# Kernel tuning notes

Hardware: AMD Instinct MI355X
Metric: run time of the kernel (lower is better)

## Reference

```python
import jax, jax.numpy as jnp
import numpy as np

E, F, H = 8, 4096, 2048  # num_experts, ffn_hidden_size, hidden_size
B, S, K = 2, 1024, 4     # batch, seq_len, top_k


def setup_inputs() -> dict:
    key = jax.random.key(0)
    ks = jax.random.split(key, 7)
    x = jax.random.normal(ks[0], (B, S, H), dtype=jnp.float32)
    weights = jax.random.uniform(ks[1], (B * S, E), dtype=jnp.float32)
    top_weights = jax.random.uniform(ks[2], (B * S, K), dtype=jnp.float32)
    top_experts = jax.random.randint(ks[3], (B * S, K), 0, E)
    w1 = jax.random.normal(ks[4], (E, F, H), dtype=jnp.float32) * 0.02
    v1 = jax.random.normal(ks[5], (E, F, H), dtype=jnp.float32) * 0.02
    w2 = jax.random.normal(ks[6], (E, F, H), dtype=jnp.float32) * 0.02
    return {"x": x, "weights": weights, "top_weights": top_weights,
            "top_experts": top_experts, "w1": w1, "v1": v1, "w2": w2}


def reference(x, weights, top_weights, top_experts, w1, v1, w2):
    # weights (router probs) is accepted but unused, matching the torch forward.
    bsz, q_len, hidden = x.shape
    xt = x.reshape(-1, hidden)  # [T, H]
    num_experts = w1.shape[0]
    # scale[t, e] = sum_k top_weights[t, k] * (top_experts[t, k] == e)
    onehot = jax.nn.one_hot(top_experts, num_experts, dtype=xt.dtype)  # [T, K, E]
    scale = jnp.einsum("tke,tk->te", onehot, top_weights)  # [T, E]
    out = jnp.zeros_like(xt)
    for e in range(num_experts):  # fixed small expert loop, dense+masked combine
        gate = xt @ w1[e].T          # [T, F]
        up = xt @ v1[e].T            # [T, F]
        h = jax.nn.silu(gate) * up   # DbrxExpertGLU
        out = out + (h @ w2[e]) * scale[:, e:e + 1]
    return out.reshape(bsz, q_len, hidden)
```

## Files before the change

kernel.cpp:

```cpp
#include <hip/hip_runtime.h>
#include <hip/hip_bf16.h>

#define NE 8
#define FF 4096
#define HH 2048
#define TT 2048
#define KTOP 4

typedef unsigned short u16;
typedef __attribute__((ext_vector_type(8))) short bf16x8;
typedef __attribute__((ext_vector_type(4))) float f32x4;

__device__ __forceinline__ u16 f2u(float f) {
  __hip_bfloat16 b = __float2bfloat16(f);
  return *reinterpret_cast<u16*>(&b);
}

__device__ __forceinline__ void gld16(void* lds, const void* g) {
  __builtin_amdgcn_global_load_lds(
      (const __attribute__((address_space(1))) void*)g,
      (__attribute__((address_space(3))) void*)lds, 16, 0, 0);
}

__global__ void k_build(const int* __restrict__ te, int* __restrict__ cnt,
                        int* __restrict__ tok, int* __restrict__ posmap) {
  const int e = blockIdx.x;
  const int tl = threadIdx.x;
  const int base = tl * 8;
  int mem[8];
  int my = 0;
  #pragma unroll
  for (int i = 0; i < 8; ++i) {
    const int t = base + i;
    bool m = false;
    #pragma unroll
    for (int k = 0; k < KTOP; ++k) m |= (te[t * KTOP + k] == e);
    mem[i] = m ? 1 : 0;
    my += mem[i];
  }
  __shared__ int s[256];
  s[tl] = my;
  __syncthreads();
  for (int off = 1; off < 256; off <<= 1) {
    int v = (tl >= off) ? s[tl - off] : 0;
    __syncthreads();
    s[tl] += v;
    __syncthreads();
  }
  int r = s[tl] - my;
  if (tl == 255) cnt[e] = s[255];
  #pragma unroll
  for (int i = 0; i < 8; ++i) {
    if (mem[i]) {
      const int t = base + i;
      tok[e * TT + r] = t;
      posmap[t * NE + e] = r;
      ++r;
    }
  }
}

__global__ void k_cast4(const float4* __restrict__ src, ushort4* __restrict__ dst, int n4) {
  int stride = gridDim.x * blockDim.x;
  for (int i = blockIdx.x * blockDim.x + threadIdx.x; i < n4; i += stride) {
    float4 f = src[i];
    ushort4 o;
    o.x = f2u(f.x); o.y = f2u(f.y); o.z = f2u(f.z); o.w = f2u(f.w);
    dst[i] = o;
  }
}

__global__ void k_tcast(const float* __restrict__ w2, u16* __restrict__ dst) {
  const int e = blockIdx.z;
  const float* src = w2 + (size_t)e * FF * HH;
  u16* d = dst + (size_t)e * HH * FF;
  __shared__ float tile[64][33];
  int h0 = blockIdx.x * 32;
  int f0 = blockIdx.y * 64;
  int tx = threadIdx.x, ty = threadIdx.y;
  #pragma unroll
  for (int i = 0; i < 8; ++i)
    tile[ty + i * 8][tx] = src[(size_t)(f0 + ty + i * 8) * HH + h0 + tx];
  __syncthreads();
  #pragma unroll
  for (int i = 0; i < 4; ++i) {
    const int hh = ty + i * 8;
    ushort2 o;
    o.x = f2u(tile[tx * 2][hh]);
    o.y = f2u(tile[tx * 2 + 1][hh]);
    *(ushort2*)&d[(size_t)(h0 + hh) * FF + f0 + tx * 2] = o;
  }
}

template<int MODE>
__global__ __launch_bounds__(512)
void gemm256(const u16* __restrict__ Aall, const u16* __restrict__ Ball,
             const int* __restrict__ cnt, void* __restrict__ Oall,
             const float* __restrict__ W1, const float* __restrict__ V1,
             const int* __restrict__ tok, const u16* __restrict__ Zp) {
  constexpr int KD  = (MODE == 0) ? HH : FF;
  constexpr int NTK = KD / 64;
  constexpr int NT  = (MODE == 0) ? 32 : 8;
  constexpr int NB  = (MODE == 0) ? 2 * FF : HH;

  const int nwg = gridDim.x;
  const int bid = blockIdx.x;
  const int swz = (bid & 7) * (nwg >> 3) + (bid >> 3);
  const int e   = swz / (8 * NT);
  const int rem = swz % (8 * NT);
  const int ntl = rem / 8;
  const int mt  = rem % 8;
  const int c = cnt[e];
  const int mcap = (c + 255) & ~255;
  if (mt * 256 >= mcap) return;

  __shared__ __align__(16) u16 smem[65536];
  const int tid  = threadIdx.x;
  const int lane = tid & 63;
  const int wave = tid >> 6;
  const int wm = wave >> 2;
  const int wn = wave & 3;

  const int tq = tid >> 2;
  const int tc = (((tid & 3) ^ ((tid >> 3) & 3)) << 3);

  const u16* pA0;
  const u16* pA1;
  if constexpr (MODE == 0) {
    const int r0 = mt * 256 + tq;
    const int r1 = r0 + 128;
    pA0 = ((r0 < c) ? Aall + (size_t)tok[e * TT + r0] * HH : Zp) + tc;
    pA1 = ((r1 < c) ? Aall + (size_t)tok[e * TT + r1] * HH : Zp) + tc;
  } else {
    const u16* A = Aall + (size_t)e * TT * KD + (size_t)(mt * 256) * KD;
    pA0 = A + (size_t)tq * KD + tc;
    pA1 = pA0 + (size_t)128 * KD;
  }

  auto stageA = [&](int d, int ks, int kt) {
    u16* dst = smem + ((d * 2 + ks) << 13) + tid * 8;
    const int off = kt * 64 + ks * 32;
    gld16(dst,        pA0 + off);
    gld16(dst + 4096, pA1 + off);
  };

  const u16* pB = Ball + (size_t)e * NB * KD + (size_t)(ntl * 256) * KD
                       + (size_t)tq * KD + tc;
  auto stageB = [&](int d, int ks, int kt) {
    u16* dst = smem + 32768 + ((d * 2 + ks) << 13) + tid * 8;
    const u16* src = pB + kt * 64 + ks * 32;
    gld16(dst,        src);
    gld16(dst + 4096, src + (size_t)128 * KD);
  };

  const float* pW = nullptr;
  if constexpr (MODE == 0) {
    const int sel = (tq >> 4) & 1;
    const int fr  = ntl * 128 + (tq >> 5) * 16 + (tq & 15);
    pW = (sel ? V1 : W1) + ((size_t)(e * FF + fr)) * HH + (tid & 3) * 8;
  }
  float4 br0[4], br1[4];
  auto issueB = [&](float4* br, int ks, int kt) {
    const float* s = pW + kt * 64 + ks * 32;
    br[0] = ((const float4*)s)[0];
    br[1] = ((const float4*)s)[1];
    const float* s2 = s + (size_t)64 * HH;
    br[2] = ((const float4*)s2)[0];
    br[3] = ((const float4*)s2)[1];
  };
  auto cvtB = [&](float4* br, int d, int ks) {
    u16* dst = smem + 32768 + ((d * 2 + ks) << 13) + tq * 32 + tc;
    union { ushort u[8]; bf16x8 v; } lo, hi;
    lo.u[0]=f2u(br[0].x); lo.u[1]=f2u(br[0].y); lo.u[2]=f2u(br[0].z); lo.u[3]=f2u(br[0].w);
    lo.u[4]=f2u(br[1].x); lo.u[5]=f2u(br[1].y); lo.u[6]=f2u(br[1].z); lo.u[7]=f2u(br[1].w);
    hi.u[0]=f2u(br[2].x); hi.u[1]=f2u(br[2].y); hi.u[2]=f2u(br[2].z); hi.u[3]=f2u(br[2].w);
    hi.u[4]=f2u(br[3].x); hi.u[5]=f2u(br[3].y); hi.u[6]=f2u(br[3].z); hi.u[7]=f2u(br[3].w);
    *(bf16x8*)(dst)        = lo.v;
    *(bf16x8*)(dst + 4096) = hi.v;
  };

  f32x4 acc[8][4];
  #pragma unroll
  for (int m = 0; m < 8; ++m)
    #pragma unroll
    for (int n = 0; n < 4; ++n)
      acc[m][n] = (f32x4){0.f, 0.f, 0.f, 0.f};

  const int lr = lane & 15;
  const int lc = ((((lane >> 4) & 3) ^ ((lane >> 1) & 3)) << 3);

  bf16x8 af[4], bf[4];
  auto rdA = [&](int d, int ks, int mq) {
    const u16* blk = smem + ((d * 2 + ks) << 13);
    #pragma unroll
    for (int m = 0; m < 4; ++m)
      af[m] = *(const bf16x8*)(blk + (wm * 128 + mq * 64 + m * 16 + lr) * 32 + lc);
  };
  auto rdB = [&](int d, int ks) {
    const u16* blk = smem + 32768 + ((d * 2 + ks) << 13);
    #pragma unroll
    for (int n = 0; n < 4; ++n)
      bf[n] = *(const bf16x8*)(blk + (wn * 64 + n * 16 + lr) * 32 + lc);
  };
  auto vmwait = [&](int n) {
    switch (n) {
      case 0:  asm volatile("s_waitcnt vmcnt(0)"  ::: "memory"); break;
      case 2:  asm volatile("s_waitcnt vmcnt(2)"  ::: "memory"); break;
      case 4:  asm volatile("s_waitcnt vmcnt(4)"  ::: "memory"); break;
      case 6:  asm volatile("s_waitcnt vmcnt(6)"  ::: "memory"); break;
      default: asm volatile("s_waitcnt vmcnt(8)"  ::: "memory"); break;
    }
  };
  auto MF = [&](int mq) {
    __builtin_amdgcn_s_setprio(1);
    #pragma unroll
    for (int m = 0; m < 4; ++m)
      #pragma unroll
      for (int n = 0; n < 4; ++n)
        acc[mq * 4 + m][n] = __builtin_amdgcn_mfma_f32_16x16x32_bf16(
            af[m], bf[n], acc[mq * 4 + m][n], 0, 0, 0);
    __builtin_amdgcn_s_setprio(0);
  };

  if constexpr (MODE == 0) {
    issueB(br0, 0, 0);
    issueB(br1, 1, 0);
    stageA(0, 0, 0);
    stageA(0, 1, 0);
    cvtB(br0, 0, 0);
    cvtB(br1, 0, 1);
    issueB(br0, 0, 1);
    issueB(br1, 1, 1);
    vmwait(8);
    asm volatile("s_waitcnt lgkmcnt(0)" ::: "memory");
  } else {
    stageA(0, 0, 0); stageB(0, 0, 0);
    stageA(0, 1, 0); stageB(0, 1, 0);
    stageA(1, 0, 1);
    vmwait(6);
  }
  __builtin_amdgcn_s_barrier();

  for (int t = 0; t < NTK; ++t) {
    const int d = t & 1, dn = d ^ 1;
    const bool hasN  = (t + 1 < NTK);
    const bool hasN2 = (t + 2 < NTK);
    rdB(d, 0); rdA(d, 0, 0);
    if constexpr (MODE == 0) { if (hasN) stageA(dn, 0, t + 1); }
    else                     { if (hasN) stageB(dn, 0, t + 1); }
    __builtin_amdgcn_s_barrier();
    asm volatile("s_waitcnt lgkmcnt(0)" ::: "memory");
    __builtin_amdgcn_sched_barrier(0);
    MF(0);
    __builtin_amdgcn_s_barrier();
    rdA(d, 0, 1);
    if (hasN) stageA(dn, 1, t + 1);
    __builtin_amdgcn_s_barrier();
    asm volatile("s_waitcnt lgkmcnt(0)" ::: "memory");
    __builtin_amdgcn_sched_barrier(0);
    MF(1);
    if constexpr (MODE == 1) {
      int v = 4 * NTK - 4 * t - 4; v = v > 3 ? 3 : (v < 0 ? 0 : v);
      vmwait(v * 2);
    }
    __builtin_amdgcn_s_barrier();
    rdB(d, 1); rdA(d, 1, 0);
    if constexpr (MODE == 1) { if (hasN) stageB(dn, 1, t + 1); }
    __builtin_amdgcn_s_barrier();
    asm volatile("s_waitcnt lgkmcnt(0)" ::: "memory");
    __builtin_amdgcn_sched_barrier(0);
    MF(0);
    if constexpr (MODE == 0) {
      if (hasN)  cvtB(br0, dn, 0);
      if (hasN2) issueB(br0, 0, t + 2);
    }
    __builtin_amdgcn_s_barrier();
    rdA(d, 1, 1);
    if constexpr (MODE == 1) { if (hasN2) stageA(d, 0, t + 2); }
    __builtin_amdgcn_s_barrier();
    asm volatile("s_waitcnt lgkmcnt(0)" ::: "memory");
    __builtin_amdgcn_sched_barrier(0);
    MF(1);
    if constexpr (MODE == 0) {
      if (hasN)  cvtB(br1, dn, 1);
      if (hasN2) issueB(br1, 1, t + 2);
      vmwait(hasN2 ? 8 : 0);
    } else {
      int v = 4 * NTK - 4 * t - 6; v = v > 3 ? 3 : (v < 0 ? 0 : v);
      vmwait(v * 2);
    }
    __builtin_amdgcn_s_barrier();
  }

  const int rb = mt * 256 + wm * 128 + ((lane >> 4) << 2);
  if (MODE == 0) {
    u16* H = (u16*)Oall + (size_t)e * TT * FF;
    const int fb = ntl * 128 + wn * 32 + lr;
    #pragma unroll
    for (int m = 0; m < 8; ++m)
      #pragma unroll
      for (int np = 0; np < 2; ++np)
        #pragma unroll
        for (int j = 0; j < 4; ++j) {
          float g = acc[m][2*np][j];
          float u = acc[m][2*np + 1][j];
          float hh = (g / (1.f + __expf(-g))) * u;
          H[(size_t)(rb + m*16 + j) * FF + fb + np*16] = f2u(hh);
        }
  } else {
    float* D = (float*)Oall + (size_t)e * TT * HH;
    const int cb = ntl * 256 + wn * 64 + lr;
    #pragma unroll
    for (int m = 0; m < 8; ++m)
      #pragma unroll
      for (int n = 0; n < 4; ++n)
        #pragma unroll
        for (int j = 0; j < 4; ++j)
          D[(size_t)(rb + m*16 + j) * HH + cb + n*16] = acc[m][n][j];
  }
}

__global__ void k_combine(const float* __restrict__ tw, const int* __restrict__ te,
                          const int* __restrict__ posmap, const float* __restrict__ dcomp,
                          float* __restrict__ out) {
  const int t = blockIdx.x;
  const int c0 = threadIdx.x * 8;
  float a[8] = {0.f, 0.f, 0.f, 0.f, 0.f, 0.f, 0.f, 0.f};
  #pragma unroll
  for (int k = 0; k < KTOP; ++k) {
    const int e = te[t * KTOP + k];
    const float w = tw[t * KTOP + k];
    const int r = posmap[t * NE + e];
    const float* row = dcomp + ((size_t)e * TT + r) * HH + c0;
    const float4 p = ((const float4*)row)[0];
    const float4 q = ((const float4*)row)[1];
    a[0] += w * p.x; a[1] += w * p.y; a[2] += w * p.z; a[3] += w * p.w;
    a[4] += w * q.x; a[5] += w * q.y; a[6] += w * q.z; a[7] += w * q.w;
  }
  float* o = out + (size_t)t * HH + c0;
  ((float4*)o)[0] = (float4){a[0], a[1], a[2], a[3]};
  ((float4*)o)[1] = (float4){a[4], a[5], a[6], a[7]};
}

extern "C" void kernel_launch(void* const* d_in, const int* in_sizes, int n_in,
                              void* d_out, int out_size, void* d_ws, size_t ws_size,
                              hipStream_t stream) {
  const float* x  = (const float*)d_in[0];
  const float* tw = (const float*)d_in[2];
  const int*   te = (const int*)d_in[3];
  const float* w1 = (const float*)d_in[4];
  const float* v1 = (const float*)d_in[5];
  const float* w2 = (const float*)d_in[6];
  float* out = (float*)d_out;

  char* p = (char*)d_ws;
  int*   cnt    = (int*)p;   p += 256;
  int*   tok    = (int*)p;   p += (size_t)NE * TT * 4;
  int*   posmap = (int*)p;   p += (size_t)TT * NE * 4;
  u16*   zp     = (u16*)p;   p += (size_t)HH * 2;
  u16*   xb     = (u16*)p;   p += (size_t)TT * HH * 2;
  u16*   w2tb   = (u16*)p;   p += (size_t)NE * HH * FF * 2;
  u16*   hc     = (u16*)p;   p += (size_t)NE * TT * FF * 2;
  float* dcomp  = (float*)p; p += (size_t)NE * TT * HH * 4;

  hipMemsetAsync(zp, 0, (size_t)HH * 2, stream);
  k_build<<<NE, 256, 0, stream>>>(te, cnt, tok, posmap);
  k_cast4<<<1024, 256, 0, stream>>>((const float4*)x, (ushort4*)xb, TT * HH / 4);
  k_tcast<<<dim3(HH / 32, FF / 64, NE), dim3(32, 8), 0, stream>>>(w2, w2tb);

  gemm256<0><<<2048, 512, 0, stream>>>(xb, w2tb, cnt, hc, w1, v1, tok, zp);
  gemm256<1><<<512, 512, 0, stream>>>(hc, w2tb, cnt, dcomp, nullptr, nullptr,
                                      nullptr, nullptr);
  k_combine<<<TT, 256, 0, stream>>>(tw, te, posmap, dcomp, out);
}
```

Measured before the change: 550.5 us.

## Fold W2 transpose-cast into GEMM1 launch and simplify main-loop barriers

```diff
diff --git a/kernel.cpp b/kernel.cpp
--- a/kernel.cpp
+++ b/kernel.cpp
@@ -10,6 +10,8 @@
 typedef unsigned short u16;
 typedef __attribute__((ext_vector_type(8))) short bf16x8;
 typedef __attribute__((ext_vector_type(4))) float f32x4;
+
+#define CFENCE asm volatile("" ::: "memory")
 
 __device__ __forceinline__ u16 f2u(float f) {
   __hip_bfloat16 b = __float2bfloat16(f);
@@ -70,42 +72,51 @@
   }
 }
 
-__global__ void k_tcast(const float* __restrict__ w2, u16* __restrict__ dst) {
-  const int e = blockIdx.z;
-  const float* src = w2 + (size_t)e * FF * HH;
-  u16* d = dst + (size_t)e * HH * FF;
-  __shared__ float tile[64][33];
-  int h0 = blockIdx.x * 32;
-  int f0 = blockIdx.y * 64;
-  int tx = threadIdx.x, ty = threadIdx.y;
-  #pragma unroll
-  for (int i = 0; i < 8; ++i)
-    tile[ty + i * 8][tx] = src[(size_t)(f0 + ty + i * 8) * HH + h0 + tx];
-  __syncthreads();
-  #pragma unroll
-  for (int i = 0; i < 4; ++i) {
-    const int hh = ty + i * 8;
-    ushort2 o;
-    o.x = f2u(tile[tx * 2][hh]);
-    o.y = f2u(tile[tx * 2 + 1][hh]);
-    *(ushort2*)&d[(size_t)(h0 + hh) * FF + f0 + tx * 2] = o;
-  }
-}
-
 template<int MODE>
 __global__ __launch_bounds__(512)
 void gemm256(const u16* __restrict__ Aall, const u16* __restrict__ Ball,
              const int* __restrict__ cnt, void* __restrict__ Oall,
              const float* __restrict__ W1, const float* __restrict__ V1,
-             const int* __restrict__ tok, const u16* __restrict__ Zp) {
+             const int* __restrict__ tok, const u16* __restrict__ Zp,
+             const float* __restrict__ W2, u16* __restrict__ W2t) {
   constexpr int KD  = (MODE == 0) ? HH : FF;
   constexpr int NTK = KD / 64;
   constexpr int NT  = (MODE == 0) ? 32 : 8;
   constexpr int NB  = (MODE == 0) ? 2 * FF : HH;
-
-  const int nwg = gridDim.x;
+  constexpr int NWG = (MODE == 0) ? 2048 : 512;
+
+  __shared__ __align__(16) u16 smem[65536];
   const int bid = blockIdx.x;
-  const int swz = (bid & 7) * (nwg >> 3) + (bid >> 3);
+  const int tid = threadIdx.x;
+
+  if (MODE == 0 && bid >= NWG) {
+    float (*tile)[65] = reinterpret_cast<float(*)[65]>(smem);
+    const int r = tid >> 3;
+    const int c0 = (tid & 7) * 8;
+    for (int i = 0; i < 8; ++i) {
+      const int g = (bid - NWG) * 8 + i;
+      const int e = g >> 11;
+      const int rem = g & 2047;
+      const int f0 = (rem >> 5) << 6;
+      const int h0 = (rem & 31) << 6;
+      const float* src = W2 + (size_t)e * FF * HH + (size_t)(f0 + r) * HH + h0 + c0;
+      float4 a = ((const float4*)src)[0];
+      float4 b = ((const float4*)src)[1];
+      tile[r][c0 + 0] = a.x; tile[r][c0 + 1] = a.y;
+      tile[r][c0 + 2] = a.z; tile[r][c0 + 3] = a.w;
+      tile[r][c0 + 4] = b.x; tile[r][c0 + 5] = b.y;
+      tile[r][c0 + 6] = b.z; tile[r][c0 + 7] = b.w;
+      __syncthreads();
+      union { ushort u[8]; bf16x8 v; } o;
+      #pragma unroll
+      for (int j = 0; j < 8; ++j) o.u[j] = f2u(tile[c0 + j][r]);
+      *(bf16x8*)(W2t + (size_t)e * HH * FF + (size_t)(h0 + r) * FF + f0 + c0) = o.v;
+      __syncthreads();
+    }
+    return;
+  }
+
+  const int swz = (bid & 7) * (NWG >> 3) + (bid >> 3);
   const int e   = swz / (8 * NT);
   const int rem = swz % (8 * NT);
   const int ntl = rem / 8;
@@ -114,8 +125,6 @@
   const int mcap = (c + 255) & ~255;
   if (mt * 256 >= mcap) return;
 
-  __shared__ __align__(16) u16 smem[65536];
-  const int tid  = threadIdx.x;
   const int lane = tid & 63;
   const int wave = tid >> 6;
   const int wm = wave >> 2;
@@ -205,8 +214,6 @@
   auto vmwait = [&](int n) {
     switch (n) {
       case 0:  asm volatile("s_waitcnt vmcnt(0)"  ::: "memory"); break;
-      case 2:  asm volatile("s_waitcnt vmcnt(2)"  ::: "memory"); break;
-      case 4:  asm volatile("s_waitcnt vmcnt(4)"  ::: "memory"); break;
       case 6:  asm volatile("s_waitcnt vmcnt(6)"  ::: "memory"); break;
       default: asm volatile("s_waitcnt vmcnt(8)"  ::: "memory"); break;
     }
@@ -234,62 +241,48 @@
     vmwait(8);
     asm volatile("s_waitcnt lgkmcnt(0)" ::: "memory");
   } else {
-    stageA(0, 0, 0); stageB(0, 0, 0);
-    stageA(0, 1, 0); stageB(0, 1, 0);
-    stageA(1, 0, 1);
-    vmwait(6);
+    stageA(0, 0, 0); stageA(0, 1, 0);
+    stageB(0, 0, 0); stageB(0, 1, 0);
+    vmwait(0);
   }
   __builtin_amdgcn_s_barrier();
+  CFENCE;
 
   for (int t = 0; t < NTK; ++t) {
     const int d = t & 1, dn = d ^ 1;
     const bool hasN  = (t + 1 < NTK);
     const bool hasN2 = (t + 2 < NTK);
+
     rdB(d, 0); rdA(d, 0, 0);
-    if constexpr (MODE == 0) { if (hasN) stageA(dn, 0, t + 1); }
-    else                     { if (hasN) stageB(dn, 0, t + 1); }
-    __builtin_amdgcn_s_barrier();
-    asm volatile("s_waitcnt lgkmcnt(0)" ::: "memory");
+    if (hasN) {
+      stageA(dn, 0, t + 1);
+      stageA(dn, 1, t + 1);
+      if constexpr (MODE == 1) { stageB(dn, 0, t + 1); stageB(dn, 1, t + 1); }
+    }
     __builtin_amdgcn_sched_barrier(0);
     MF(0);
-    __builtin_amdgcn_s_barrier();
     rdA(d, 0, 1);
-    if (hasN) stageA(dn, 1, t + 1);
-    __builtin_amdgcn_s_barrier();
-    asm volatile("s_waitcnt lgkmcnt(0)" ::: "memory");
-    __builtin_amdgcn_sched_barrier(0);
     MF(1);
-    if constexpr (MODE == 1) {
-      int v = 4 * NTK - 4 * t - 4; v = v > 3 ? 3 : (v < 0 ? 0 : v);
-      vmwait(v * 2);
-    }
-    __builtin_amdgcn_s_barrier();
-    rdB(d, 1); rdA(d, 1, 0);
-    if constexpr (MODE == 1) { if (hasN) stageB(dn, 1, t + 1); }
-    __builtin_amdgcn_s_barrier();
-    asm volatile("s_waitcnt lgkmcnt(0)" ::: "memory");
-    __builtin_amdgcn_sched_barrier(0);
-    MF(0);
     if constexpr (MODE == 0) {
       if (hasN)  cvtB(br0, dn, 0);
       if (hasN2) issueB(br0, 0, t + 2);
     }
-    __builtin_amdgcn_s_barrier();
-    rdA(d, 1, 1);
-    if constexpr (MODE == 1) { if (hasN2) stageA(d, 0, t + 2); }
-    __builtin_amdgcn_s_barrier();
-    asm volatile("s_waitcnt lgkmcnt(0)" ::: "memory");
-    __builtin_amdgcn_sched_barrier(0);
-    MF(1);
+    rdB(d, 1); rdA(d, 1, 0);
+    MF(0);
     if constexpr (MODE == 0) {
       if (hasN)  cvtB(br1, dn, 1);
       if (hasN2) issueB(br1, 1, t + 2);
+    }
+    rdA(d, 1, 1);
+    MF(1);
+    if constexpr (MODE == 0) {
+      asm volatile("s_waitcnt lgkmcnt(0)" ::: "memory");
       vmwait(hasN2 ? 8 : 0);
     } else {
-      int v = 4 * NTK - 4 * t - 6; v = v > 3 ? 3 : (v < 0 ? 0 : v);
-      vmwait(v * 2);
+      vmwait(0);
     }
     __builtin_amdgcn_s_barrier();
+    CFENCE;
   }
 
   const int rb = mt * 256 + wm * 128 + ((lane >> 4) << 2);
@@ -366,10 +359,10 @@
   hipMemsetAsync(zp, 0, (size_t)HH * 2, stream);
   k_build<<<NE, 256, 0, stream>>>(te, cnt, tok, posmap);
   k_cast4<<<1024, 256, 0, stream>>>((const float4*)x, (ushort4*)xb, TT * HH / 4);
-  k_tcast<<<dim3(HH / 32, FF / 64, NE), dim3(32, 8), 0, stream>>>(w2, w2tb);
-
-  gemm256<0><<<2048, 512, 0, stream>>>(xb, w2tb, cnt, hc, w1, v1, tok, zp);
+
+  gemm256<0><<<4096, 512, 0, stream>>>(xb, nullptr, cnt, hc, w1, v1, tok, zp,
+                                       w2, w2tb);
   gemm256<1><<<512, 512, 0, stream>>>(hc, w2tb, cnt, dcomp, nullptr, nullptr,
-                                      nullptr, nullptr);
+                                      nullptr, nullptr, nullptr, nullptr);
   k_combine<<<TT, 256, 0, stream>>>(tw, te, posmap, dcomp, out);
 }
```

Measured after the change: 507.5 us. 7.8% less time.
